# Performance work log

Hardware: AMD Instinct MI355X
Metric: run time of the kernel (lower is better)

Reference implementation:

```python
import jax, jax.numpy as jnp
import numpy as np

B, C, L, D = 8, 256, 2048, 128  # batch, in_channels, seq_len, n_factor


def setup_inputs() -> dict:
    key = jax.random.key(0)
    ks = jax.random.split(key, 8)
    s = 1.0 / np.sqrt(C)
    return {
        "x_inner": jax.random.normal(ks[0], (B, C, L), jnp.float32),
        "x_outer": jax.random.normal(ks[1], (B, C, L), jnp.float32),
        "Wq": jax.random.normal(ks[2], (D, C), jnp.float32) * s,
        "bq": jax.random.normal(ks[3], (D,), jnp.float32) * 0.01,
        "Wk": jax.random.normal(ks[4], (D, C), jnp.float32) * s,
        "bk": jax.random.normal(ks[5], (D,), jnp.float32) * 0.01,
        "Wv": jax.random.normal(ks[6], (D, C), jnp.float32) * s,
        "bv": jax.random.normal(ks[7], (D,), jnp.float32) * 0.01,
    }


def reference(x_inner, x_outer, Wq, bq, Wk, bk, Wv, bv):
    # kernel-size-1 Conv1d == per-position linear over channels; permute -> [B, L, D]
    q = jnp.einsum('bcl,dc->bld', x_inner, Wq) + bq  # [B, Lq, D]
    k = jnp.einsum('bcl,dc->bld', x_outer, Wk) + bk  # [B, Lk, D]
    v = jnp.einsum('bcl,dc->bld', x_outer, Wv) + bv  # [B, Lk, D]
    scores = jnp.einsum('bqd,bkd->bqk', q, k) / jnp.sqrt(jnp.asarray(D, q.dtype))
    attn = jax.nn.softmax(scores, axis=2)            # [B, Lq, Lk]
    return jnp.einsum('bqk,bkd->bqd', attn, v)       # [B, Lq, D]
```

## Files before the change

kernel.cpp:

```cpp
#include <hip/hip_runtime.h>
#include <hip/hip_bf16.h>

#define NB 8
#define NC 256
#define NL 2048
#define ND 128
#define NROWS (NB * NL)
#define QKV_ELEMS ((size_t)NB * NL * ND)
#define W_ELEMS (ND * NC)
#define XS_STRIDE 264

typedef __attribute__((ext_vector_type(8))) short bf16x8;
typedef __attribute__((ext_vector_type(4))) float f32x4;
typedef __attribute__((ext_vector_type(16))) float f32x16;

__device__ __forceinline__ unsigned short f2bf(float f) {
    union { float f; unsigned u; } v; v.f = f;
    unsigned r = v.u + 0x7fffu + ((v.u >> 16) & 1u);
    return (unsigned short)(r >> 16);
}

__device__ __forceinline__ void load_lds16(const unsigned short* g, unsigned short* l) {
    __builtin_amdgcn_global_load_lds((const __attribute__((address_space(1))) unsigned int*)g,
                                     (__attribute__((address_space(3))) unsigned int*)l, 16, 0, 0);
}

__global__ void cast_w3(const float* __restrict__ wq, const float* __restrict__ wk,
                        const float* __restrict__ wv, unsigned short* __restrict__ dst) {
    int i = blockIdx.x * blockDim.x + threadIdx.x;
    if (i >= 3 * W_ELEMS) return;
    int sel = i / W_ELEMS, off = i - sel * W_ELEMS;
    const float* s = (sel == 0) ? wq : (sel == 1) ? wk : wv;
    dst[i] = f2bf(s[off]);
}

__global__ __launch_bounds__(256, 4) void proj_direct(const float* __restrict__ xi,
                                                      const float* __restrict__ xo,
                                                      const unsigned short* __restrict__ Wall,
                                                      const float* __restrict__ bq,
                                                      const float* __restrict__ bk,
                                                      const float* __restrict__ bv,
                                                      unsigned short* __restrict__ Qb,
                                                      unsigned short* __restrict__ Kb,
                                                      unsigned short* __restrict__ Vtb) {
    __shared__ unsigned short xs[64 * XS_STRIDE];
    int b = blockIdx.x >> 5, lt = blockIdx.x & 31, l0 = lt * 64;
    int y = blockIdx.y;
    int wave = threadIdx.x >> 6, lane = threadIdx.x & 63;
    int ln = lane & 15, quad = lane >> 4;

    const float* xsrc = (y == 0 ? xi : xo) + (size_t)b * NC * NL + l0;
    int l4 = (lane & 15) * 4;
    int cr0 = wave * 4 + (lane >> 4);
    #pragma unroll
    for (int g = 0; g < 4; g++) {
        float4 r[4];
        #pragma unroll
        for (int gi = 0; gi < 4; gi++) {
            int c = cr0 + (g * 4 + gi) * 16;
            r[gi] = *reinterpret_cast<const float4*>(xsrc + (size_t)c * NL + l4);
        }
        #pragma unroll
        for (int gi = 0; gi < 4; gi++) {
            int c = cr0 + (g * 4 + gi) * 16;
            xs[(l4 + 0) * XS_STRIDE + c] = f2bf(r[gi].x);
            xs[(l4 + 1) * XS_STRIDE + c] = f2bf(r[gi].y);
            xs[(l4 + 2) * XS_STRIDE + c] = f2bf(r[gi].z);
            xs[(l4 + 3) * XS_STRIDE + c] = f2bf(r[gi].w);
        }
    }
    __syncthreads();

    if (y < 2) {
        const unsigned short* Wb = Wall + (size_t)y * W_ELEMS;
        const float* bias = y ? bk : bq;
        unsigned short* out = y ? Kb : Qb;
        int m0w = wave * 16;
        f32x4 acc[8] = {};
        #pragma unroll
        for (int s = 0; s < 8; s++) {
            bf16x8 af = *reinterpret_cast<const bf16x8*>(xs + (m0w + ln) * XS_STRIDE + s * 32 + quad * 8);
            #pragma unroll
            for (int t = 0; t < 8; t++) {
                bf16x8 bfr = *reinterpret_cast<const bf16x8*>(Wb + (size_t)(t * 16 + ln) * NC + s * 32 + quad * 8);
                acc[t] = __builtin_amdgcn_mfma_f32_16x16x32_bf16(af, bfr, acc[t], 0, 0, 0);
            }
        }
        #pragma unroll
        for (int t = 0; t < 8; t++) {
            int col = t * 16 + ln;
            float bi = bias[col];
            #pragma unroll
            for (int r = 0; r < 4; r++)
                out[(size_t)(b * NL + l0 + m0w + quad * 4 + r) * ND + col] = f2bf(acc[t][r] + bi);
        }
    } else {
        const unsigned short* Wb = Wall + 2 * (size_t)W_ELEMS;
        f32x4 acc[2][4] = {};
        #pragma unroll
        for (int s = 0; s < 8; s++) {
            bf16x8 wf0 = *reinterpret_cast<const bf16x8*>(Wb + (size_t)(wave * 32 + ln) * NC + s * 32 + quad * 8);
            bf16x8 wf1 = *reinterpret_cast<const bf16x8*>(Wb + (size_t)(wave * 32 + 16 + ln) * NC + s * 32 + quad * 8);
            #pragma unroll
            for (int t = 0; t < 4; t++) {
                bf16x8 xb = *reinterpret_cast<const bf16x8*>(xs + (t * 16 + ln) * XS_STRIDE + s * 32 + quad * 8);
                acc[0][t] = __builtin_amdgcn_mfma_f32_16x16x32_bf16(wf0, xb, acc[0][t], 0, 0, 0);
                acc[1][t] = __builtin_amdgcn_mfma_f32_16x16x32_bf16(wf1, xb, acc[1][t], 0, 0, 0);
            }
        }
        #pragma unroll
        for (int u = 0; u < 2; u++)
            #pragma unroll
            for (int t = 0; t < 4; t++)
                #pragma unroll
                for (int r = 0; r < 4; r++) {
                    int d = wave * 32 + u * 16 + quad * 4 + r;
                    Vtb[(size_t)(b * ND + d) * NL + l0 + t * 16 + ln] = f2bf(acc[u][t][r] + bv[d]);
                }
    }
}

__global__ __launch_bounds__(256, 2) void flash_attn_split(const unsigned short* __restrict__ Q,
                                                           const unsigned short* __restrict__ K,
                                                           const unsigned short* __restrict__ Vt,
                                                           float* __restrict__ Opart,
                                                           float* __restrict__ lbuf,
                                                           int kvlen) {
    __shared__ unsigned short kbuf[2][64 * 128];
    __shared__ unsigned short vbuf[2][128 * 64];
    __shared__ unsigned short pbuf[4][32 * 64];
    int b = blockIdx.x >> 4, qt = blockIdx.x & 15;
    int sp = blockIdx.y;
    int kv0 = sp * kvlen;
    int wave = threadIdx.x >> 6, lane = threadIdx.x & 63;
    int l31 = lane & 31, h = lane >> 5;
    int m0 = qt * 128 + wave * 32;
    const float scale = 0.08838834764831845f * 1.4426950408889634f;

    bf16x8 qf[8];
    const unsigned short* qrow = Q + (size_t)(b * NL + m0 + l31) * ND + h * 8;
    #pragma unroll
    for (int s = 0; s < 8; s++) qf[s] = *reinterpret_cast<const bf16x8*>(qrow + s * 16);

    float lsum = 0.f;
    f32x16 o_acc[4] = {};

    unsigned short* pw = pbuf[wave];
    const unsigned short* kg = K + (size_t)b * NL * ND;
    const unsigned short* vg = Vt + (size_t)b * ND * NL;

    int krt = wave * 16 + (lane >> 4);
    int kjs = (lane & 15);
    int vdt = wave * 32 + (lane >> 3);
    int vjs = (lane & 7);

    {
        int kt = kv0;
        #pragma unroll
        for (int i = 0; i < 4; i++) {
            int rt = krt + i * 4;
            load_lds16(kg + (size_t)(kt + rt) * ND + (kjs ^ (rt & 15)) * 8, kbuf[0] + (wave * 16 + i * 4) * 128);
        }
        #pragma unroll
        for (int i = 0; i < 4; i++) {
            int dt = vdt + i * 8;
            load_lds16(vg + (size_t)dt * NL + kt + (vjs ^ (dt & 7)) * 8, vbuf[0] + (wave * 32 + i * 8) * 64);
        }
    }

    int niter = kvlen >> 6;
    for (int it = 0; it < niter; it++) {
        int cur = it & 1;
        __syncthreads();

        if (it + 1 < niter) {
            int kt = kv0 + (it + 1) * 64;
            int nxt = cur ^ 1;
            #pragma unroll
            for (int i = 0; i < 4; i++) {
                int rt = krt + i * 4;
                load_lds16(kg + (size_t)(kt + rt) * ND + (kjs ^ (rt & 15)) * 8, kbuf[nxt] + (wave * 16 + i * 4) * 128);
            }
            #pragma unroll
            for (int i = 0; i < 4; i++) {
                int dt = vdt + i * 8;
                load_lds16(vg + (size_t)dt * NL + kt + (vjs ^ (dt & 7)) * 8, vbuf[nxt] + (wave * 32 + i * 8) * 64);
            }
        }
        const unsigned short* kb = kbuf[cur];
        const unsigned short* vb = vbuf[cur];

        f32x16 sacc[2] = {};
        #pragma unroll
        for (int tt = 0; tt < 2; tt++) {
            const unsigned short* krow_p = kb + (tt * 32 + l31) * 128;
            #pragma unroll
            for (int s = 0; s < 8; s++) {
                bf16x8 kf = *reinterpret_cast<const bf16x8*>(krow_p + (((s * 2 + h) ^ (lane & 15)) << 3));
                sacc[tt] = __builtin_amdgcn_mfma_f32_32x32x16_bf16(kf, qf[s], sacc[tt], 0, 0, 0);
            }
        }
        #pragma unroll
        for (int tt = 0; tt < 2; tt++) {
            #pragma unroll
            for (int g = 0; g < 4; g++) {
                float p0 = __builtin_exp2f(sacc[tt][g * 4 + 0] * scale);
                float p1 = __builtin_exp2f(sacc[tt][g * 4 + 1] * scale);
                float p2 = __builtin_exp2f(sacc[tt][g * 4 + 2] * scale);
                float p3 = __builtin_exp2f(sacc[tt][g * 4 + 3] * scale);
                lsum += (p0 + p1) + (p2 + p3);
                ushort4 o4 = { f2bf(p0), f2bf(p1), f2bf(p2), f2bf(p3) };
                int chunk = tt * 4 + g;
                *reinterpret_cast<ushort4*>(pw + l31 * 64 + ((chunk ^ (l31 & 7)) << 3) + h * 4) = o4;
            }
        }
        bf16x8 pb[4];
        #pragma unroll
        for (int step = 0; step < 4; step++)
            pb[step] = *reinterpret_cast<const bf16x8*>(pw + l31 * 64 + (((step * 2 + h) ^ (l31 & 7)) << 3));
        #pragma unroll
        for (int dt = 0; dt < 4; dt++) {
            const unsigned short* vrow = vb + (dt * 32 + l31) * 64;
            #pragma unroll
            for (int step = 0; step < 4; step++) {
                bf16x8 vf = *reinterpret_cast<const bf16x8*>(vrow + (((step * 2 + h) ^ (l31 & 7)) << 3));
                o_acc[dt] = __builtin_amdgcn_mfma_f32_32x32x16_bf16(vf, pb[step], o_acc[dt], 0, 0, 0);
            }
        }
    }
    lsum += __shfl_xor(lsum, 32);

    float* op = Opart + (size_t)sp * QKV_ELEMS;
    int qrow_g = b * NL + m0 + l31;
    if (lane < 32) lbuf[(size_t)sp * NROWS + qrow_g] = lsum;
    #pragma unroll
    for (int dt = 0; dt < 4; dt++) {
        #pragma unroll
        for (int g = 0; g < 4; g++) {
            f32x4 v4 = { o_acc[dt][g * 4 + 0], o_acc[dt][g * 4 + 1],
                         o_acc[dt][g * 4 + 2], o_acc[dt][g * 4 + 3] };
            *reinterpret_cast<f32x4*>(op + (size_t)qrow_g * ND + dt * 32 + g * 8 + h * 4) = v4;
        }
    }
}

__global__ __launch_bounds__(256) void attn_merge(const float* __restrict__ Opart,
                                                  const float* __restrict__ lbuf,
                                                  float* __restrict__ out, int S) {
    int idx = blockIdx.x * 256 + threadIdx.x;
    int row = idx >> 5;
    int dg = (idx & 31) * 4;
    float L = 0.f;
    float4 acc = make_float4(0.f, 0.f, 0.f, 0.f);
    for (int s = 0; s < S; s++) {
        L += lbuf[(size_t)s * NROWS + row];
        float4 o = *reinterpret_cast<const float4*>(Opart + (size_t)s * QKV_ELEMS + (size_t)row * ND + dg);
        acc.x += o.x; acc.y += o.y; acc.z += o.z; acc.w += o.w;
    }
    float inv = 1.0f / L;
    float4 res = make_float4(acc.x * inv, acc.y * inv, acc.z * inv, acc.w * inv);
    *reinterpret_cast<float4*>(out + (size_t)row * ND + dg) = res;
}

extern "C" void kernel_launch(void* const* d_in, const int* in_sizes, int n_in,
                              void* d_out, int out_size, void* d_ws, size_t ws_size,
                              hipStream_t stream) {
    const float* x_inner = (const float*)d_in[0];
    const float* x_outer = (const float*)d_in[1];
    const float* Wq = (const float*)d_in[2];
    const float* bq = (const float*)d_in[3];
    const float* Wk = (const float*)d_in[4];
    const float* bk = (const float*)d_in[5];
    const float* Wv = (const float*)d_in[6];
    const float* bv = (const float*)d_in[7];
    float* out = (float*)d_out;

    size_t need4 = 34078720u + 3 * QKV_ELEMS * 2 + 3 * W_ELEMS * 2;
    int S = (ws_size >= need4) ? 4 : 2;
    size_t union_bytes = (S == 4) ? 34078720u : 17039360u;

    char* w = (char*)d_ws;
    float* Opart = (float*)w;
    float* lbuf = (float*)(w + (size_t)S * QKV_ELEMS * 4);
    unsigned short* Qb = (unsigned short*)(w + union_bytes);
    unsigned short* Kb = Qb + QKV_ELEMS;
    unsigned short* Vtb = Kb + QKV_ELEMS;
    unsigned short* Wall = Vtb + QKV_ELEMS;

    cast_w3<<<(3 * W_ELEMS + 255) / 256, 256, 0, stream>>>(Wq, Wk, Wv, Wall);
    dim3 pgrid(NB * (NL / 64), 3);
    proj_direct<<<pgrid, 256, 0, stream>>>(x_inner, x_outer, Wall, bq, bk, bv, Qb, Kb, Vtb);
    dim3 fgrid(NB * (NL / 128), S);
    flash_attn_split<<<fgrid, 256, 0, stream>>>(Qb, Kb, Vtb, Opart, lbuf, NL / S);
    attn_merge<<<(NROWS * ND / 4 + 255) / 256, 256, 0, stream>>>(Opart, lbuf, out, S);
}
```

Baseline: 149.3 us.

## Keep softmax probabilities in registers via permlane32 swap instead of LDS round-trip

Builds the P operand for the PV MFMA directly in registers. The exp results are packed with v_cvt_pk_bf16_f32 and exchanged between half-waves with v_permlane32_swap, which removes the per-wave LDS pbuf write and read-back. It also remaps blockIdx so that neighbouring blocks spread across batches, and raises wave priority around the MFMA sections with s_setprio. The register shuffle has to match the MFMA B-operand layout exactly, and the block remap changes how the K/V working set lands in L2.

Result: no change. 147.3 us (-1.4%).

```diff
diff --git a/kernel.cpp b/kernel.cpp
--- a/kernel.cpp
+++ b/kernel.cpp
@@ -13,11 +13,22 @@
 typedef __attribute__((ext_vector_type(8))) short bf16x8;
 typedef __attribute__((ext_vector_type(4))) float f32x4;
 typedef __attribute__((ext_vector_type(16))) float f32x16;
+typedef __attribute__((ext_vector_type(4))) unsigned int u32x4;
 
 __device__ __forceinline__ unsigned short f2bf(float f) {
     union { float f; unsigned u; } v; v.f = f;
     unsigned r = v.u + 0x7fffu + ((v.u >> 16) & 1u);
     return (unsigned short)(r >> 16);
+}
+
+__device__ __forceinline__ unsigned cvt_pk_bf16(float lo, float hi) {
+    unsigned r;
+    asm("v_cvt_pk_bf16_f32 %0, %1, %2" : "=v"(r) : "v"(lo), "v"(hi));
+    return r;
+}
+
+__device__ __forceinline__ void pl32swap(unsigned &a, unsigned &b) {
+    asm("v_permlane32_swap_b32 %0, %1" : "+v"(a), "+v"(b));
 }
 
 __device__ __forceinline__ void load_lds16(const unsigned short* g, unsigned short* l) {
@@ -128,8 +139,9 @@
                                                            int kvlen) {
     __shared__ unsigned short kbuf[2][64 * 128];
     __shared__ unsigned short vbuf[2][128 * 64];
-    __shared__ unsigned short pbuf[4][32 * 64];
-    int b = blockIdx.x >> 4, qt = blockIdx.x & 15;
+    int bx = blockIdx.x;
+    bx = ((bx & 7) << 4) | (bx >> 3);
+    int b = bx >> 4, qt = bx & 15;
     int sp = blockIdx.y;
     int kv0 = sp * kvlen;
     int wave = threadIdx.x >> 6, lane = threadIdx.x & 63;
@@ -145,7 +157,6 @@
     float lsum = 0.f;
     f32x16 o_acc[4] = {};
 
-    unsigned short* pw = pbuf[wave];
     const unsigned short* kg = K + (size_t)b * NL * ND;
     const unsigned short* vg = Vt + (size_t)b * ND * NL;
 
@@ -191,6 +202,7 @@
         const unsigned short* vb = vbuf[cur];
 
         f32x16 sacc[2] = {};
+        __builtin_amdgcn_s_setprio(1);
         #pragma unroll
         for (int tt = 0; tt < 2; tt++) {
             const unsigned short* krow_p = kb + (tt * 32 + l31) * 128;
@@ -200,24 +212,29 @@
                 sacc[tt] = __builtin_amdgcn_mfma_f32_32x32x16_bf16(kf, qf[s], sacc[tt], 0, 0, 0);
             }
         }
+        __builtin_amdgcn_s_setprio(0);
+
+        bf16x8 pb[4];
         #pragma unroll
         for (int tt = 0; tt < 2; tt++) {
-            #pragma unroll
-            for (int g = 0; g < 4; g++) {
-                float p0 = __builtin_exp2f(sacc[tt][g * 4 + 0] * scale);
-                float p1 = __builtin_exp2f(sacc[tt][g * 4 + 1] * scale);
-                float p2 = __builtin_exp2f(sacc[tt][g * 4 + 2] * scale);
-                float p3 = __builtin_exp2f(sacc[tt][g * 4 + 3] * scale);
-                lsum += (p0 + p1) + (p2 + p3);
-                ushort4 o4 = { f2bf(p0), f2bf(p1), f2bf(p2), f2bf(p3) };
-                int chunk = tt * 4 + g;
-                *reinterpret_cast<ushort4*>(pw + l31 * 64 + ((chunk ^ (l31 & 7)) << 3) + h * 4) = o4;
-            }
-        }
-        bf16x8 pb[4];
-        #pragma unroll
-        for (int step = 0; step < 4; step++)
-            pb[step] = *reinterpret_cast<const bf16x8*>(pw + l31 * 64 + (((step * 2 + h) ^ (l31 & 7)) << 3));
+            float p[16];
+            #pragma unroll
+            for (int g = 0; g < 16; g++) p[g] = __builtin_exp2f(sacc[tt][g] * scale);
+            lsum += (((p[0] + p[1]) + (p[2] + p[3])) + ((p[4] + p[5]) + (p[6] + p[7])))
+                  + (((p[8] + p[9]) + (p[10] + p[11])) + ((p[12] + p[13]) + (p[14] + p[15])));
+            unsigned c0 = cvt_pk_bf16(p[0], p[1]),   c1 = cvt_pk_bf16(p[2], p[3]);
+            unsigned c2 = cvt_pk_bf16(p[4], p[5]),   c3 = cvt_pk_bf16(p[6], p[7]);
+            unsigned c4 = cvt_pk_bf16(p[8], p[9]),   c5 = cvt_pk_bf16(p[10], p[11]);
+            unsigned c6 = cvt_pk_bf16(p[12], p[13]), c7 = cvt_pk_bf16(p[14], p[15]);
+            pl32swap(c0, c2); pl32swap(c1, c3);
+            pl32swap(c4, c6); pl32swap(c5, c7);
+            u32x4 wlo = {c0, c1, c2, c3};
+            u32x4 whi = {c4, c5, c6, c7};
+            pb[tt * 2]     = __builtin_bit_cast(bf16x8, wlo);
+            pb[tt * 2 + 1] = __builtin_bit_cast(bf16x8, whi);
+        }
+
+        __builtin_amdgcn_s_setprio(1);
         #pragma unroll
         for (int dt = 0; dt < 4; dt++) {
             const unsigned short* vrow = vb + (dt * 32 + l31) * 64;
@@ -227,6 +244,7 @@
                 o_acc[dt] = __builtin_amdgcn_mfma_f32_32x32x16_bf16(vf, pb[step], o_acc[dt], 0, 0, 0);
             }
         }
+        __builtin_amdgcn_s_setprio(0);
     }
     lsum += __shfl_xor(lsum, 32);
 
```
